# Optimization experiments

Hardware: AMD Instinct MI355X
Metric: run time of the kernel (lower is better)

## Reference

```python
import jax, jax.numpy as jnp
import numpy as np
from jax.scipy.linalg import expm

B, T, DIM = 8, 4096, 256


def setup_inputs() -> dict:
    key = jax.random.key(0)
    k1, k2 = jax.random.split(key)
    psi = jax.random.normal(k1, (B, T, 4, DIM), dtype=jnp.float32)
    H = jax.random.normal(k2, (4, DIM, DIM), dtype=jnp.float32) * 0.02
    return {"psi": psi, "H": H}


def reference(psi, H):
    # H_complex = H[0] + i*H[1]; components H[2], H[3] are unused (as in the torch code)
    H_complex = (H[0] + 1j * H[1]).astype(jnp.complex64)
    # Unitary-like evolution operator U = expm(-i * H_complex), [dim, dim] complex64
    U = expm(-1j * H_complex)
    # All 4 quaternion components share the same U -> one batched complex matmul
    psi_c = psi.astype(jnp.complex64)  # [B, T, 4, dim]
    evolved = jnp.einsum('btcd,de->btce', psi_c, U)  # complex matmul over last dim
    # Torch code keeps only the real part of each evolved component
    return evolved.real.astype(jnp.float32)
```

## Files before the change

kernel.cpp:

```cpp
#include <hip/hip_runtime.h>
#include <hip/hip_bf16.h>

#define NDIM 256
#define NN (NDIM*NDIM)

typedef __attribute__((ext_vector_type(8))) short s8bf;
typedef __attribute__((ext_vector_type(4))) float f32x4;

__device__ __forceinline__ unsigned short f2bf(float f) {
    union { float f; unsigned u; } v; v.f = f;
    unsigned u = v.u;
    return (unsigned short)((u + 0x7FFFu + ((u >> 16) & 1u)) >> 16);
}
__device__ __forceinline__ short f2bfs(float f) {
    __hip_bfloat16 h = __float2bfloat16(f);
    union { __hip_bfloat16 h; short s; } v; v.h = h;
    return v.s;
}

__global__ __launch_bounds__(1024) void kmm(
    const float* __restrict__ H, float2* __restrict__ M2c, float2* __restrict__ M3c,
    unsigned short* __restrict__ Ut, int mode) {
    __shared__ float2 As[16][257];
    __shared__ float2 Bs[256][17];
    __shared__ float2 Rs[3][16][17];
    const int tx = threadIdx.x, ty = threadIdx.y, tz = threadIdx.z;
    const int tid = (tz * 16 + ty) * 16 + tx;
    const int r0 = blockIdx.y * 16, c0 = blockIdx.x * 16;

#pragma unroll
    for (int i = 0; i < 4; ++i) {
        int idx = i * 1024 + tid;
        int r = idx >> 8, k = idx & 255;
        float2 a;
        if (mode == 0)      { a.x = H[NN + (r0+r)*NDIM + k]; a.y = -H[(r0+r)*NDIM + k]; }
        else if (mode == 1) a = M2c[(r0+r)*NDIM + k];
        else                a = M3c[(r0+r)*NDIM + k];
        As[r][k] = a;
    }
#pragma unroll
    for (int i = 0; i < 4; ++i) {
        int idx = i * 1024 + tid;
        int k = idx >> 4, cc = idx & 15;
        float2 b;
        if (mode <= 1) { b.x = H[NN + k*NDIM + c0+cc]; b.y = -H[k*NDIM + c0+cc]; }
        else {
            int g = k * NDIM + c0 + cc;
            float mr = H[NN + g], mi = -H[g];
            float2 m2 = M2c[g], m3 = M3c[g];
            float di = (k == c0 + cc) ? 1.f : 0.f;
            b.x = di*(1.f/6.f) + mr*(1.f/24.f) + m2.x*(1.f/120.f) + m3.x*(1.f/720.f);
            b.y =                mi*(1.f/24.f) + m2.y*(1.f/120.f) + m3.y*(1.f/720.f);
        }
        Bs[k][cc] = b;
    }
    __syncthreads();

    float sr0=0.f, si0=0.f, sr1=0.f, si1=0.f;
#pragma unroll 8
    for (int k = tz*64; k < tz*64 + 64; k += 2) {
        float2 a = As[ty][k], b = Bs[k][tx];
        sr0 = fmaf(a.x, b.x, sr0); sr0 = fmaf(-a.y, b.y, sr0);
        si0 = fmaf(a.x, b.y, si0); si0 = fmaf(a.y, b.x, si0);
        float2 a1 = As[ty][k+1], b1 = Bs[k+1][tx];
        sr1 = fmaf(a1.x, b1.x, sr1); sr1 = fmaf(-a1.y, b1.y, sr1);
        si1 = fmaf(a1.x, b1.y, si1); si1 = fmaf(a1.y, b1.x, si1);
    }
    float sr = sr0 + sr1, si = si0 + si1;
    if (tz > 0) Rs[tz-1][ty][tx] = make_float2(sr, si);
    __syncthreads();
    if (tz == 0) {
        sr += Rs[0][ty][tx].x + Rs[1][ty][tx].x + Rs[2][ty][tx].x;
        si += Rs[0][ty][tx].y + Rs[1][ty][tx].y + Rs[2][ty][tx].y;
        int d = r0 + ty, e = c0 + tx;
        if (mode == 0)      M2c[d*NDIM + e] = make_float2(sr, si);
        else if (mode == 1) M3c[d*NDIM + e] = make_float2(sr, si);
        else {
            int g = d * NDIM + e;
            float ur = sr + ((d == e) ? 1.f : 0.f) + H[NN + g] + M2c[g].x * 0.5f;
            Ut[e * NDIM + d] = f2bf(ur);
        }
    }
}

__global__ __launch_bounds__(512, 1) void kgemm(
    const float* __restrict__ psi, const unsigned short* __restrict__ Ut,
    float* __restrict__ out) {
    __shared__ unsigned short Bls[NN];
    __shared__ float Escr[8][512];
    const int t = threadIdx.x;

    const s8bf* Ug = (const s8bf*)Ut;
    s8bf* Bg = (s8bf*)Bls;
#pragma unroll
    for (int i = 0; i < 16; ++i) {
        int g = i * 512 + t;
        int r = g >> 5, j = g & 31;
        Bg[(r << 5) | (j ^ (r & 7))] = Ug[g];
    }
    __syncthreads();

    const int w = t >> 6, lane = t & 63;
    const int c = lane & 15, q = lane >> 4;
    const f32x4* psi4 = (const f32x4*)psi;
    f32x4* out4 = (f32x4*)out;
    float* Ebase = &Escr[w][0];

    size_t rl = ((size_t)blockIdx.x * 512 + w * 16 + c) * 64;

    f32x4 pb[8][2];
#pragma unroll
    for (int s = 0; s < 8; ++s) {
        pb[s][0] = psi4[rl + s * 8 + q * 2];
        pb[s][1] = psi4[rl + s * 8 + q * 2 + 1];
    }

#pragma unroll 1
    for (int st = 0; st < 4; ++st) {
        const int baserow = blockIdx.x * 512 + st * 128 + w * 16;
        const size_t rln = rl + (size_t)128 * 64;

        f32x4 acc[16];
#pragma unroll
        for (int i = 0; i < 16; ++i) acc[i] = (f32x4)0.f;

#pragma unroll
        for (int s = 0; s < 8; ++s) {
            s8bf a;
#pragma unroll
            for (int j = 0; j < 4; ++j) {
                a[j]     = f2bfs(pb[s][0][j]);
                a[j + 4] = f2bfs(pb[s][1][j]);
            }
            if (st < 3) {
                pb[s][0] = psi4[rln + s * 8 + q * 2];
                pb[s][1] = psi4[rln + s * 8 + q * 2 + 1];
            }
#pragma unroll
            for (int ct = 0; ct < 16; ++ct) {
                int rr = ct * 16 + c;
                s8bf bb = Bg[(rr << 5) | ((s * 4 + q) ^ (rr & 7))];
                acc[ct] = __builtin_amdgcn_mfma_f32_16x16x32_bf16(a, bb, acc[ct], 0, 0, 0);
            }
        }
        rl = rln;

#pragma unroll
        for (int p = 0; p < 16; ++p) {
            const int qq = p >> 2, rr = p & 3;
            float* E = Ebase + (p & 1) * 256;
            if (q == qq) {
#pragma unroll
                for (int ct = 0; ct < 16; ++ct)
                    E[ct * 16 + c] = acc[ct][rr];
            }
            f32x4 vv = *(const f32x4*)(&E[lane * 4]);
            __builtin_nontemporal_store(vv, &out4[(size_t)(baserow + p) * 64 + lane]);
            __builtin_amdgcn_sched_barrier(0);
        }
    }
}

extern "C" void kernel_launch(void* const* d_in, const int* in_sizes, int n_in,
                              void* d_out, int out_size, void* d_ws, size_t ws_size,
                              hipStream_t stream) {
    const float* psi = (const float*)d_in[0];
    const float* H   = (const float*)d_in[1];
    float* out = (float*)d_out;

    float2* M2c = (float2*)d_ws;
    float2* M3c = M2c + NN;
    unsigned short* Ut = (unsigned short*)(M3c + NN);

    dim3 cb(16, 16, 4), cg(16, 16);
    kmm<<<cg, cb, 0, stream>>>(H, M2c, M3c, Ut, 0);
    kmm<<<cg, cb, 0, stream>>>(H, M2c, M3c, Ut, 1);
    kmm<<<cg, cb, 0, stream>>>(H, M2c, M3c, Ut, 2);
    kgemm<<<256, 512, 0, stream>>>(psi, Ut, out);
}
```

Measured before the change: 74.59 us.

## Software-pipeline GEMM stages with ping-pong accumulators and interleaved epilogue stores

The kgemm main loop is fully unrolled into four row-stages that alternate between two accumulator sets. The output epilogue of the previous stage is interleaved with the MFMA steps of the current stage, so stores overlap with matrix math. The psi prefetch buffer shrinks from an 8-step to a 2-step ring loaded just ahead of use, freeing registers for the second accumulator. The cost is more register pressure and code size from the double accumulators, and less prefetch distance for the psi loads.

```diff
diff --git a/kernel.cpp b/kernel.cpp
--- a/kernel.cpp
+++ b/kernel.cpp
@@ -83,6 +83,46 @@
     }
 }
 
+__device__ __forceinline__ void main_step(
+    int s, const f32x4* psi4, const s8bf* Bg, int c, int q,
+    size_t rl, size_t rlN, f32x4 pb[2][2], f32x4 acc[16]) {
+    s8bf a;
+#pragma unroll
+    for (int j = 0; j < 4; ++j) {
+        a[j]     = f2bfs(pb[s & 1][0][j]);
+        a[j + 4] = f2bfs(pb[s & 1][1][j]);
+    }
+    if (s < 6) {
+        int o = (s + 2) * 8 + q * 2;
+        pb[s & 1][0] = psi4[rl + o];
+        pb[s & 1][1] = psi4[rl + o + 1];
+    } else {
+        int o = (s - 6) * 8 + q * 2;
+        pb[s & 1][0] = psi4[rlN + o];
+        pb[s & 1][1] = psi4[rlN + o + 1];
+    }
+#pragma unroll
+    for (int ct = 0; ct < 16; ++ct) {
+        int rr = ct * 16 + c;
+        s8bf bb = Bg[(rr << 5) | ((s * 4 + q) ^ (rr & 7))];
+        acc[ct] = __builtin_amdgcn_mfma_f32_16x16x32_bf16(a, bb, acc[ct], 0, 0, 0);
+    }
+}
+
+__device__ __forceinline__ void epi_pass(
+    int p, int c, int q, int lane, float* Ebase, const f32x4 acc[16],
+    f32x4* out4, int baseP) {
+    const int qq = p >> 2, rr = p & 3;
+    float* E = Ebase + (p & 1) * 256;
+    if (q == qq) {
+#pragma unroll
+        for (int ct = 0; ct < 16; ++ct) E[ct * 16 + c] = acc[ct][rr];
+    }
+    f32x4 vv = *(const f32x4*)(&E[lane * 4]);
+    __builtin_nontemporal_store(vv, &out4[(size_t)(baseP + p) * 64 + lane]);
+    __builtin_amdgcn_sched_barrier(0);
+}
+
 __global__ __launch_bounds__(512, 1) void kgemm(
     const float* __restrict__ psi, const unsigned short* __restrict__ Ut,
     float* __restrict__ out) {
@@ -106,59 +146,52 @@
     f32x4* out4 = (f32x4*)out;
     float* Ebase = &Escr[w][0];
 
-    size_t rl = ((size_t)blockIdx.x * 512 + w * 16 + c) * 64;
-
-    f32x4 pb[8][2];
+    const int bb0 = blockIdx.x * 512 + w * 16;
+    const size_t rl0 = (size_t)(bb0 +       c) * 64;
+    const size_t rl1 = (size_t)(bb0 + 128 + c) * 64;
+    const size_t rl2 = (size_t)(bb0 + 256 + c) * 64;
+    const size_t rl3 = (size_t)(bb0 + 384 + c) * 64;
+
+    f32x4 accA[16], accB[16], pb[2][2];
+
+    pb[0][0] = psi4[rl0 + q*2];     pb[0][1] = psi4[rl0 + q*2 + 1];
+    pb[1][0] = psi4[rl0 + 8 + q*2]; pb[1][1] = psi4[rl0 + 8 + q*2 + 1];
+
+#pragma unroll
+    for (int i = 0; i < 16; ++i) accA[i] = (f32x4)0.f;
+#pragma unroll
+    for (int s = 0; s < 8; ++s) main_step(s, psi4, Bg, c, q, rl0, rl1, pb, accA);
+
+#pragma unroll
+    for (int i = 0; i < 16; ++i) accB[i] = (f32x4)0.f;
 #pragma unroll
     for (int s = 0; s < 8; ++s) {
-        pb[s][0] = psi4[rl + s * 8 + q * 2];
-        pb[s][1] = psi4[rl + s * 8 + q * 2 + 1];
-    }
-
-#pragma unroll 1
-    for (int st = 0; st < 4; ++st) {
-        const int baserow = blockIdx.x * 512 + st * 128 + w * 16;
-        const size_t rln = rl + (size_t)128 * 64;
-
-        f32x4 acc[16];
-#pragma unroll
-        for (int i = 0; i < 16; ++i) acc[i] = (f32x4)0.f;
-
-#pragma unroll
-        for (int s = 0; s < 8; ++s) {
-            s8bf a;
-#pragma unroll
-            for (int j = 0; j < 4; ++j) {
-                a[j]     = f2bfs(pb[s][0][j]);
-                a[j + 4] = f2bfs(pb[s][1][j]);
-            }
-            if (st < 3) {
-                pb[s][0] = psi4[rln + s * 8 + q * 2];
-                pb[s][1] = psi4[rln + s * 8 + q * 2 + 1];
-            }
-#pragma unroll
-            for (int ct = 0; ct < 16; ++ct) {
-                int rr = ct * 16 + c;
-                s8bf bb = Bg[(rr << 5) | ((s * 4 + q) ^ (rr & 7))];
-                acc[ct] = __builtin_amdgcn_mfma_f32_16x16x32_bf16(a, bb, acc[ct], 0, 0, 0);
-            }
-        }
-        rl = rln;
-
-#pragma unroll
-        for (int p = 0; p < 16; ++p) {
-            const int qq = p >> 2, rr = p & 3;
-            float* E = Ebase + (p & 1) * 256;
-            if (q == qq) {
-#pragma unroll
-                for (int ct = 0; ct < 16; ++ct)
-                    E[ct * 16 + c] = acc[ct][rr];
-            }
-            f32x4 vv = *(const f32x4*)(&E[lane * 4]);
-            __builtin_nontemporal_store(vv, &out4[(size_t)(baserow + p) * 64 + lane]);
-            __builtin_amdgcn_sched_barrier(0);
-        }
-    }
+        main_step(s, psi4, Bg, c, q, rl1, rl2, pb, accB);
+        epi_pass(2*s,     c, q, lane, Ebase, accA, out4, bb0);
+        epi_pass(2*s + 1, c, q, lane, Ebase, accA, out4, bb0);
+    }
+
+#pragma unroll
+    for (int i = 0; i < 16; ++i) accA[i] = (f32x4)0.f;
+#pragma unroll
+    for (int s = 0; s < 8; ++s) {
+        main_step(s, psi4, Bg, c, q, rl2, rl3, pb, accA);
+        epi_pass(2*s,     c, q, lane, Ebase, accB, out4, bb0 + 128);
+        epi_pass(2*s + 1, c, q, lane, Ebase, accB, out4, bb0 + 128);
+    }
+
+#pragma unroll
+    for (int i = 0; i < 16; ++i) accB[i] = (f32x4)0.f;
+#pragma unroll
+    for (int s = 0; s < 8; ++s) {
+        main_step(s, psi4, Bg, c, q, rl3, rl3, pb, accB);
+        epi_pass(2*s,     c, q, lane, Ebase, accA, out4, bb0 + 256);
+        epi_pass(2*s + 1, c, q, lane, Ebase, accA, out4, bb0 + 256);
+    }
+
+#pragma unroll
+    for (int p = 0; p < 16; ++p)
+        epi_pass(p, c, q, lane, Ebase, accB, out4, bb0 + 384);
 }
 
 extern "C" void kernel_launch(void* const* d_in, const int* in_sizes, int n_in,
```

New measurement: 76.59 us. +2.7%, slower.
